# Optimization experiments

Measured on AMD Instinct MI355X. Metric: run time of the kernel, lower is better.

## Reference

```python
import jax, jax.numpy as jnp
import numpy as np

B, T, D = 8, 2048, 128        # batch, time, input_dim
C, CD = 8192, 128             # codebook_size, codebook_dim
COMMIT_W = 1.0                # commitment_weight
IN2Q_W = 0.25                 # input_to_quantize_commit_loss_weight
EPS = 1e-12


def setup_inputs() -> dict:
    key = jax.random.key(0)
    k = jax.random.split(key, 4)
    z = jax.random.normal(k[0], (B, T, D), jnp.float32)
    frozen_codebook = jax.random.normal(k[1], (C, CD), jnp.float32) * CD ** -0.5
    conv_v = jax.random.normal(k[2], (D, CD), jnp.float32) * CD ** -0.5  # weight-norm direction (1x1 conv weight squeezed)
    conv_g = jnp.linalg.norm(conv_v, axis=1)                             # weight-norm gain (torch init: g = ||v||)
    conv_b = jnp.zeros((D,), jnp.float32)
    return {"z": z, "frozen_codebook": frozen_codebook, "conv_v": conv_v,
            "conv_g": conv_g, "conv_b": conv_b}


def _implicit_codebook(fc, v, g, b):
    # weight-normed 1x1 conv == linear: w = g * v / ||v||_row ; out = fc @ w.T + b
    w = g[:, None] * v / jnp.linalg.norm(v, axis=1, keepdims=True)
    return fc @ w.T + b  # (C, D)


def _rotate_to(src, tgt):
    # rotation trick (Fifty et al.): Householder-style rotation, grads flow only through src
    sg = jax.lax.stop_gradient
    norm_src = jnp.linalg.norm(src, axis=-1, keepdims=True)
    norm_tgt = jnp.linalg.norm(tgt, axis=-1, keepdims=True)
    u = sg(src / jnp.maximum(norm_src, EPS))
    q = sg(tgt / jnp.maximum(norm_tgt, EPS))
    w = u + q
    w = sg(w / jnp.maximum(jnp.linalg.norm(w, axis=-1, keepdims=True), EPS))
    e = src
    rotated = (e
               - 2.0 * jnp.sum(e * w, -1, keepdims=True) * w
               + 2.0 * jnp.sum(e * u, -1, keepdims=True) * q)
    scale = sg(norm_tgt / jnp.maximum(norm_src, EPS))
    return rotated * scale


def reference(z, frozen_codebook, conv_v, conv_g, conv_b):
    sg = jax.lax.stop_gradient
    cb = _implicit_codebook(frozen_codebook, conv_v, conv_g, conv_b)  # (C, D)
    # squared euclidean distances -> same argmin as torch.cdist (p=2)
    d2 = (jnp.sum(z * z, -1, keepdims=True)
          - 2.0 * jnp.einsum('btd,cd->btc', z, cb)
          + jnp.sum(cb * cb, -1))                                     # (B, T, C)
    indices = jnp.argmin(d2, axis=-1)                                 # (B, T)
    z_q = cb[indices]                                                 # (B, T, D)
    commit = (jnp.mean((sg(z) - z_q) ** 2)
              + IN2Q_W * jnp.mean((z - sg(z_q)) ** 2))
    z_q = _rotate_to(z, z_q)
    return z_q, indices, commit * COMMIT_W
```

## Files before the change

kernel.cpp:

```cpp
#include <hip/hip_runtime.h>
#include <math.h>

#define NROWS 16384
#define DIM 128
#define NCODE 8192
#define EPSF 1e-12f

typedef float f32x4 __attribute__((ext_vector_type(4)));
typedef __bf16 bf16x8 __attribute__((ext_vector_type(8)));
typedef unsigned short u16x8 __attribute__((ext_vector_type(8)));

#define WS_NEED_BYTES 31571968ull

#define KT 12
#define TILEA 4096
#define TILEB 8192
#define KPB 3
#define CHUNK (TILEA + TILEB)

__device__ __forceinline__ float wave_sum(float x) {
#pragma unroll
  for (int off = 32; off > 0; off >>= 1) x += __shfl_xor(x, off, 64);
  return x;
}

__device__ __forceinline__ unsigned short f2bf(float x) {
  union { float f; unsigned int u; } v;
  v.f = x;
  unsigned int r = v.u + 0x7fffu + ((v.u >> 16) & 1u);
  return (unsigned short)(r >> 16);
}
__device__ __forceinline__ float bf2f(unsigned short h) {
  union { float f; unsigned int u; } v;
  v.u = ((unsigned int)h) << 16;
  return v.f;
}

__device__ __forceinline__ void gload_lds16(const unsigned short* g,
                                            unsigned short* l) {
  __builtin_amdgcn_global_load_lds(
      (const __attribute__((address_space(1))) void*)g,
      (__attribute__((address_space(3))) void*)l, 16, 0, 0);
}

__global__ void wprep_kernel(const float* __restrict__ v,
                             const float* __restrict__ g,
                             float* __restrict__ Wt) {
  const int d = blockIdx.x;
  const int lane = threadIdx.x;
  const float v0 = v[d * DIM + lane], v1 = v[d * DIM + lane + 64];
  const float ss = wave_sum(fmaf(v0, v0, v1 * v1));
  const float sc = g[d] / sqrtf(ss);
  Wt[lane * DIM + d] = v0 * sc;
  Wt[(lane + 64) * DIM + d] = v1 * sc;
}

__global__ __launch_bounds__(256, 2) void codebook_kernel(
    const float* __restrict__ fc, const float* __restrict__ Wt,
    const float* __restrict__ bias, float* __restrict__ cb,
    float* __restrict__ cnorm2, unsigned short* __restrict__ cbcat) {
  __shared__ float Ws[DIM][DIM];
  const int tid = threadIdx.x;
  for (int i = tid; i < 4096; i += 256)
    *(float4*)&Ws[0][i << 2] = *(const float4*)&Wt[i << 2];
  __syncthreads();

  const int lane = tid & 63, wid = tid >> 6;
  const int c0 = blockIdx.x * 16 + wid * 4;
  const float b0 = bias[lane], b1 = bias[lane + 64];

  for (int cc = 0; cc < 4; ++cc) {
    const int c = __builtin_amdgcn_readfirstlane(c0 + cc);
    float a0 = 0.f, a1 = 0.f;
    for (int k = 0; k < DIM; k += 4) {
      const float4 f4 = *(const float4*)&fc[c * DIM + k];
      a0 = fmaf(f4.x, Ws[k][lane], a0);
      a1 = fmaf(f4.x, Ws[k][lane + 64], a1);
      a0 = fmaf(f4.y, Ws[k + 1][lane], a0);
      a1 = fmaf(f4.y, Ws[k + 1][lane + 64], a1);
      a0 = fmaf(f4.z, Ws[k + 2][lane], a0);
      a1 = fmaf(f4.z, Ws[k + 2][lane + 64], a1);
      a0 = fmaf(f4.w, Ws[k + 3][lane], a0);
      a1 = fmaf(f4.w, Ws[k + 3][lane + 64], a1);
    }
    const float o0 = a0 + b0, o1 = a1 + b1;
    cb[c * DIM + lane] = o0;
    cb[c * DIM + lane + 64] = o1;
    const float ss = wave_sum(fmaf(o0, o0, o1 * o1));
    if (lane == 0) cnorm2[c] = ss;

    if (cbcat != nullptr) {
      const int ct = c >> 8, r = c & 255;
      const unsigned int swz = ((r >> 1) & 3) << 3;
      unsigned short* base = cbcat + (size_t)ct * (KT * TILEB);
#pragma unroll
      for (int h = 0; h < 2; ++h) {
        const int d = lane + 64 * h;
        const float val = h ? o1 : o0;
        const unsigned short hi = f2bf(val);
        const unsigned short lo = f2bf(val - bf2f(hi));
        const int ktl = d >> 5;
        const int off = (r << 5) + ((d & 31) ^ swz);
        base[ktl * TILEB + off] = hi;
        base[(4 + ktl) * TILEB + off] = lo;
        base[(8 + ktl) * TILEB + off] = hi;
      }
    }
  }
}

__global__ __launch_bounds__(256) void zprep_kernel(
    const float* __restrict__ z, unsigned short* __restrict__ zcat) {
  const int id = blockIdx.x * 256 + threadIdx.x;
  const int row = id / 48, s = id - row * 48;
  const int kt = s >> 2, s4 = s & 3;
  const int seg = kt >> 2;
  const int d0 = ((kt & 3) << 5) + (s4 << 3);
  const int r = row & 127, rt = row >> 7;
  const int slotsw = s4 ^ ((r >> 1) & 3);

  const float* zp = &z[(size_t)row * DIM + d0];
  u16x8 out;
#pragma unroll
  for (int i = 0; i < 8; ++i) {
    const float x = zp[i];
    unsigned short b = f2bf(x);
    if (seg == 2) b = f2bf(x - bf2f(b));
    out[i] = b;
  }
  *(u16x8*)&zcat[(size_t)(rt * KT + kt) * TILEA + (r << 5) + (slotsw << 3)] =
      out;
}

__global__ __launch_bounds__(512, 4) void mfma_argmin_kernel(
    const unsigned short* __restrict__ zcat,
    const unsigned short* __restrict__ cbcat,
    const float* __restrict__ cnorm2, float* __restrict__ pval,
    int* __restrict__ pidx) {
  __shared__ __align__(16) unsigned short S[KPB * CHUNK];

  const int xcd = blockIdx.x & 7, idx = blockIdx.x >> 3;
  const int rt = xcd * 16 + (idx & 15);
  const int ct = idx >> 4;

  const int tid = threadIdx.x;
  const int lane = tid & 63, wid = tid >> 6;
  const int wr = wid >> 2, wc = wid & 3;
  const int l15 = lane & 15, lg = lane >> 4;
  const int tid8 = tid * 8;

  const unsigned short* Ag = zcat + (size_t)rt * (KT * TILEA);
  const unsigned short* Bg = cbcat + (size_t)ct * (KT * TILEB);

  f32x4 acc[4][4];
#pragma unroll
  for (int mi = 0; mi < 4; ++mi)
#pragma unroll
    for (int ni = 0; ni < 4; ++ni) acc[mi][ni] = f32x4{0.f, 0.f, 0.f, 0.f};

  int aoff[4], boff[4];
#pragma unroll
  for (int i = 0; i < 4; ++i) {
    const int ra = wr * 64 + i * 16 + l15;
    aoff[i] = (ra << 5) + ((lg ^ ((ra >> 1) & 3)) << 3);
    const int rc = wc * 64 + i * 16 + l15;
    boff[i] = TILEA + (rc << 5) + ((lg ^ ((rc >> 1) & 3)) << 3);
  }

  for (int it = 0; it < KT / KPB; ++it) {
    __syncthreads();
#pragma unroll
    for (int kk = 0; kk < KPB; ++kk) {
      const int kt = it * KPB + kk;
      gload_lds16(Ag + kt * TILEA + tid8, &S[kk * CHUNK + tid8]);
      gload_lds16(Bg + kt * TILEB + tid8, &S[kk * CHUNK + TILEA + tid8]);
      gload_lds16(Bg + kt * TILEB + 4096 + tid8,
                  &S[kk * CHUNK + TILEA + 4096 + tid8]);
    }
    __syncthreads();

#pragma unroll
    for (int kk = 0; kk < KPB; ++kk) {
      const int sb = kk * CHUNK;
      bf16x8 af[4], bfr[4];
#pragma unroll
      for (int i = 0; i < 4; ++i) af[i] = *(const bf16x8*)&S[sb + aoff[i]];
#pragma unroll
      for (int i = 0; i < 4; ++i) bfr[i] = *(const bf16x8*)&S[sb + boff[i]];
#pragma unroll
      for (int mi = 0; mi < 4; ++mi)
#pragma unroll
        for (int ni = 0; ni < 4; ++ni)
          acc[mi][ni] = __builtin_amdgcn_mfma_f32_16x16x32_bf16(
              af[mi], bfr[ni], acc[mi][ni], 0, 0, 0);
    }
  }
  __syncthreads();

  float* exv = (float*)&S[0];
  int* exi = (int*)&S[2048];

  float cn[4];
#pragma unroll
  for (int ni = 0; ni < 4; ++ni)
    cn[ni] = cnorm2[ct * 256 + wc * 64 + ni * 16 + l15];

#pragma unroll
  for (int mi = 0; mi < 4; ++mi) {
#pragma unroll
    for (int rg = 0; rg < 4; ++rg) {
      float bv = 3.4e38f;
      int bi = 0;
#pragma unroll
      for (int ni = 0; ni < 4; ++ni) {
        const float d = fmaf(-2.f, acc[mi][ni][rg], cn[ni]);
        if (d < bv) { bv = d; bi = ct * 256 + wc * 64 + ni * 16 + l15; }
      }
#pragma unroll
      for (int off = 1; off < 16; off <<= 1) {
        const float ov = __shfl_xor(bv, off, 64);
        const int oi = __shfl_xor(bi, off, 64);
        if (ov < bv || (ov == bv && oi < bi)) { bv = ov; bi = oi; }
      }
      if (l15 == 0) {
        const int rloc = wr * 64 + mi * 16 + (lg << 2) + rg;
        exv[wc * 128 + rloc] = bv;
        exi[wc * 128 + rloc] = bi;
      }
    }
  }
  __syncthreads();
  if (tid < 128) {
    float bv = exv[tid];
    int bi = exi[tid];
#pragma unroll
    for (int w = 1; w < 4; ++w) {
      const float v = exv[w * 128 + tid];
      if (v < bv) { bv = v; bi = exi[w * 128 + tid]; }
    }
    const int row = rt * 128 + tid;
    pval[(size_t)ct * NROWS + row] = bv;
    pidx[(size_t)ct * NROWS + row] = bi;
  }
}

__global__ __launch_bounds__(256, 1) void argmin_kernel(
    const float* __restrict__ z, const float* __restrict__ cb,
    const float* __restrict__ cnorm2, float* __restrict__ pval,
    int* __restrict__ pidx) {
  __shared__ float zs[128][DIM];
  __shared__ float cs[128][DIM];

  const int tid = threadIdx.x;
  const int rb = blockIdx.x >> 1;
  const int ch = blockIdx.x & 1;
  const int row0 = rb * 128;
  const int code0 = ch * (NCODE / 2);

  for (int i = tid; i < 128 * 32; i += 256) {
    const int r = i >> 5, f = i & 31;
    *(float4*)&zs[r][f << 2] = *(const float4*)&z[(row0 + r) * DIM + (f << 2)];
  }

  const int tx = tid & 15, ty = tid >> 4;
  const int sw = tx & 7;

  float best[8];
  int besti[8];
#pragma unroll
  for (int r = 0; r < 8; ++r) { best[r] = 3.4e38f; besti[r] = 0; }

  for (int cc = 0; cc < NCODE / 2; cc += 128) {
    __syncthreads();
    for (int i = tid; i < 128 * 32; i += 256) {
      const int r = i >> 5, f = i & 31;
      const int fg = f ^ (r & 7);
      *(float4*)&cs[r][f << 2] =
          *(const float4*)&cb[(code0 + cc + r) * DIM + (fg << 2)];
    }
    __syncthreads();

    float acc[8][8];
#pragma unroll
    for (int r = 0; r < 8; ++r)
#pragma unroll
      for (int j = 0; j < 8; ++j) acc[r][j] = 0.f;

    for (int k = 0; k < DIM; k += 4) {
      const int f = k >> 2;
      float4 zr[8], cr[8];
#pragma unroll
      for (int r = 0; r < 8; ++r) zr[r] = *(const float4*)&zs[ty + 16 * r][k];
      const int col = ((f ^ sw) << 2);
#pragma unroll
      for (int j = 0; j < 8; ++j) cr[j] = *(const float4*)&cs[tx + 16 * j][col];
#pragma unroll
      for (int r = 0; r < 8; ++r)
#pragma unroll
        for (int j = 0; j < 8; ++j) {
          acc[r][j] = fmaf(zr[r].x, cr[j].x, acc[r][j]);
          acc[r][j] = fmaf(zr[r].y, cr[j].y, acc[r][j]);
          acc[r][j] = fmaf(zr[r].z, cr[j].z, acc[r][j]);
          acc[r][j] = fmaf(zr[r].w, cr[j].w, acc[r][j]);
        }
    }

#pragma unroll
    for (int j = 0; j < 8; ++j) {
      const int code = code0 + cc + tx + 16 * j;
      const float cnv = cnorm2[code];
#pragma unroll
      for (int r = 0; r < 8; ++r) {
        const float s = fmaf(-2.f, acc[r][j], cnv);
        if (s < best[r]) { best[r] = s; besti[r] = code; }
      }
    }
  }

#pragma unroll
  for (int off = 1; off < 16; off <<= 1) {
#pragma unroll
    for (int r = 0; r < 8; ++r) {
      const float ov = __shfl_xor(best[r], off, 64);
      const int oi = __shfl_xor(besti[r], off, 64);
      if (ov < best[r] || (ov == best[r] && oi < besti[r])) {
        best[r] = ov;
        besti[r] = oi;
      }
    }
  }
  if (tx == 0) {
#pragma unroll
    for (int r = 0; r < 8; ++r) {
      const int row = row0 + ty + 16 * r;
      pval[(size_t)ch * NROWS + row] = best[r];
      pidx[(size_t)ch * NROWS + row] = besti[r];
    }
  }
}

__global__ __launch_bounds__(256) void rotate_kernel(
    const float* __restrict__ z, const float* __restrict__ cb,
    const float* __restrict__ pval, const int* __restrict__ pidx, int ntiles,
    float* __restrict__ out_zq, float* __restrict__ out_idx,
    float* __restrict__ partials) {
  const int tid = threadIdx.x;
  const int wid = tid >> 6, lane = tid & 63;
  const int row = blockIdx.x * 4 + wid;

  float bv = 3.4e38f;
  int bi = 0x7fffffff;
  if (lane < ntiles) {
    bv = pval[(size_t)lane * NROWS + row];
    bi = pidx[(size_t)lane * NROWS + row];
  }
#pragma unroll
  for (int off = 32; off > 0; off >>= 1) {
    const float ov = __shfl_xor(bv, off, 64);
    const int oi = __shfl_xor(bi, off, 64);
    if (ov < bv || (ov == bv && oi < bi)) { bv = ov; bi = oi; }
  }
  const int ci = bi;

  const float z0 = z[row * DIM + lane], z1 = z[row * DIM + lane + 64];
  const float c0 = cb[ci * DIM + lane], c1 = cb[ci * DIM + lane + 64];

  const float ns2 = wave_sum(fmaf(z0, z0, z1 * z1));
  const float nt2 = wave_sum(fmaf(c0, c0, c1 * c1));
  const float ns = sqrtf(ns2), nt = sqrtf(nt2);
  const float dns = fmaxf(ns, EPSF), dnt = fmaxf(nt, EPSF);
  const float u0 = z0 / dns, u1 = z1 / dns;
  const float q0 = c0 / dnt, q1 = c1 / dnt;
  float w0 = u0 + q0, w1 = u1 + q1;
  const float nw = sqrtf(wave_sum(fmaf(w0, w0, w1 * w1)));
  const float dnw = fmaxf(nw, EPSF);
  w0 /= dnw;
  w1 /= dnw;
  const float ew = wave_sum(fmaf(z0, w0, z1 * w1));
  const float eu = wave_sum(fmaf(z0, u0, z1 * u1));
  const float sc = nt / dns;
  const float o0 = (z0 - 2.f * ew * w0 + 2.f * eu * q0) * sc;
  const float o1 = (z1 - 2.f * ew * w1 + 2.f * eu * q1) * sc;
  out_zq[row * DIM + lane] = o0;
  out_zq[row * DIM + lane + 64] = o1;
  if (lane == 0) out_idx[row] = (float)ci;

  const float d0 = z0 - c0, d1 = z1 - c1;
  const float rsum = wave_sum(fmaf(d0, d0, d1 * d1));
  __shared__ float pr[4];
  if (lane == 0) pr[wid] = rsum;
  __syncthreads();
  if (tid == 0) partials[blockIdx.x] = (pr[0] + pr[1]) + (pr[2] + pr[3]);
}

__global__ void finalize_kernel(const float* __restrict__ partials,
                                float* __restrict__ out_commit) {
  __shared__ float red[256];
  const int tid = threadIdx.x;
  float s = 0.f;
  for (int i = tid; i < 4096; i += 256) s += partials[i];
  red[tid] = s;
  __syncthreads();
  for (int off = 128; off > 0; off >>= 1) {
    if (tid < off) red[tid] += red[tid + off];
    __syncthreads();
  }
  if (tid == 0) out_commit[0] = red[0] * (1.25f / ((float)NROWS * (float)DIM));
}

extern "C" void kernel_launch(void* const* d_in, const int* in_sizes, int n_in,
                              void* d_out, int out_size, void* d_ws,
                              size_t ws_size, hipStream_t stream) {
  const float* z = (const float*)d_in[0];
  const float* fc = (const float*)d_in[1];
  const float* conv_v = (const float*)d_in[2];
  const float* conv_g = (const float*)d_in[3];
  const float* conv_b = (const float*)d_in[4];
  float* out = (float*)d_out;

  float* ws = (float*)d_ws;
  float* cb = ws;
  float* cnorm2 = ws + 1048576;
  float* Wt = ws + 1056768;

  if (ws_size >= WS_NEED_BYTES) {
    unsigned short* zcat = (unsigned short*)(ws + 1073152);
    unsigned short* cbcat = (unsigned short*)(ws + 4218880);
    float* pval = ws + 5791744;
    int* pidx = (int*)(ws + 6840320);
    float* partials = ws + 7888896;

    wprep_kernel<<<DIM, 64, 0, stream>>>(conv_v, conv_g, Wt);
    codebook_kernel<<<NCODE / 16, 256, 0, stream>>>(fc, Wt, conv_b, cb, cnorm2,
                                                    cbcat);
    zprep_kernel<<<NROWS * 48 / 256, 256, 0, stream>>>(z, zcat);
    mfma_argmin_kernel<<<4096, 512, 0, stream>>>(zcat, cbcat, cnorm2, pval,
                                                 pidx);
    rotate_kernel<<<NROWS / 4, 256, 0, stream>>>(z, cb, pval, pidx, 32, out,
                                                 out + 2097152, partials);
    finalize_kernel<<<1, 256, 0, stream>>>(partials, out + 2113536);
  } else {
    float* pval = ws + 1073152;
    int* pidx = (int*)(ws + 1105920);
    float* partials = ws + 1138688;

    wprep_kernel<<<DIM, 64, 0, stream>>>(conv_v, conv_g, Wt);
    codebook_kernel<<<NCODE / 16, 256, 0, stream>>>(fc, Wt, conv_b, cb, cnorm2,
                                                    nullptr);
    argmin_kernel<<<256, 256, 0, stream>>>(z, cb, cnorm2, pval, pidx);
    rotate_kernel<<<NROWS / 4, 256, 0, stream>>>(z, cb, pval, pidx, 2, out,
                                                 out + 2097152, partials);
    finalize_kernel<<<1, 256, 0, stream>>>(partials, out + 2113536);
  }
}
```

Before: 212.1 us.

## Switch argmin to 32x32 MFMA, atomic packed argmin, fuse prep and finalize kernels

Replaces the 16x16x32 MFMA tiling with 32x32x16 bf16 MFMA (2x2 accumulators of 16 floats per wave), which halves the LDS fragment loads per MFMA. Per-tile partial argmin results are now combined via a 64-bit atomicMin on an order-preserving packed (value,index) key instead of writing pval/pidx arrays that the rotate kernel had to reduce. The z-prep and weight-norm prep kernels are merged into one launch that also initialises the atomic buffers. The commit-loss finalize kernel is removed in favour of fixed-point atomic accumulation with a last-block-done counter in the rotate kernel. Together these cut kernel launches and global traffic, at the cost of atomics contention and a fixed-point approximation of the loss sum.

```diff
diff --git a/kernel.cpp b/kernel.cpp
--- a/kernel.cpp
+++ b/kernel.cpp
@@ -7,6 +7,7 @@
 #define EPSF 1e-12f
 
 typedef float f32x4 __attribute__((ext_vector_type(4)));
+typedef float f32x16 __attribute__((ext_vector_type(16)));
 typedef __bf16 bf16x8 __attribute__((ext_vector_type(8)));
 typedef unsigned short u16x8 __attribute__((ext_vector_type(8)));
 
@@ -43,16 +44,47 @@
       (__attribute__((address_space(3))) void*)l, 16, 0, 0);
 }
 
-__global__ void wprep_kernel(const float* __restrict__ v,
-                             const float* __restrict__ g,
-                             float* __restrict__ Wt) {
-  const int d = blockIdx.x;
-  const int lane = threadIdx.x;
-  const float v0 = v[d * DIM + lane], v1 = v[d * DIM + lane + 64];
-  const float ss = wave_sum(fmaf(v0, v0, v1 * v1));
-  const float sc = g[d] / sqrtf(ss);
-  Wt[lane * DIM + d] = v0 * sc;
-  Wt[(lane + 64) * DIM + d] = v1 * sc;
+__global__ __launch_bounds__(256) void wz_kernel(
+    const float* __restrict__ z, const float* __restrict__ v,
+    const float* __restrict__ g, unsigned short* __restrict__ zcat,
+    float* __restrict__ Wt, unsigned long long* __restrict__ amin,
+    unsigned long long* __restrict__ sumdev, unsigned* __restrict__ cntdev) {
+  const int b = blockIdx.x;
+  if (b < 3072) {
+    const int id = b * 256 + threadIdx.x;
+    const int row = id / 48, s = id - row * 48;
+    if (s == 0) amin[row] = ~0ull;
+    if (id == 0) {
+      atomicExch(sumdev, 0ull);
+      atomicExch(cntdev, 0u);
+    }
+    const int kt = s >> 2, s4 = s & 3;
+    const int seg = kt >> 2;
+    const int d0 = ((kt & 3) << 5) + (s4 << 3);
+    const int r = row & 127, rt = row >> 7;
+    const int slotsw = s4 ^ ((r >> 1) & 3);
+
+    const float* zp = &z[(size_t)row * DIM + d0];
+    u16x8 out;
+#pragma unroll
+    for (int i = 0; i < 8; ++i) {
+      const float x = zp[i];
+      unsigned short bb = f2bf(x);
+      if (seg == 2) bb = f2bf(x - bf2f(bb));
+      out[i] = bb;
+    }
+    *(u16x8*)&zcat[(size_t)(rt * KT + kt) * TILEA + (r << 5) + (slotsw << 3)] =
+        out;
+  } else {
+    const int tid = threadIdx.x;
+    const int wid = tid >> 6, lane = tid & 63;
+    const int d = (b - 3072) * 4 + wid;
+    const float v0 = v[d * DIM + lane], v1 = v[d * DIM + lane + 64];
+    const float ss = wave_sum(fmaf(v0, v0, v1 * v1));
+    const float sc = g[d] / sqrtf(ss);
+    Wt[lane * DIM + d] = v0 * sc;
+    Wt[(lane + 64) * DIM + d] = v1 * sc;
+  }
 }
 
 __global__ __launch_bounds__(256, 2) void codebook_kernel(
@@ -97,46 +129,23 @@
       for (int h = 0; h < 2; ++h) {
         const int d = lane + 64 * h;
         const float val = h ? o1 : o0;
-        const unsigned short hi = f2bf(val);
-        const unsigned short lo = f2bf(val - bf2f(hi));
+        const unsigned short hiv = f2bf(val);
+        const unsigned short lov = f2bf(val - bf2f(hiv));
         const int ktl = d >> 5;
         const int off = (r << 5) + ((d & 31) ^ swz);
-        base[ktl * TILEB + off] = hi;
-        base[(4 + ktl) * TILEB + off] = lo;
-        base[(8 + ktl) * TILEB + off] = hi;
+        base[ktl * TILEB + off] = hiv;
+        base[(4 + ktl) * TILEB + off] = lov;
+        base[(8 + ktl) * TILEB + off] = hiv;
       }
     }
   }
-}
-
-__global__ __launch_bounds__(256) void zprep_kernel(
-    const float* __restrict__ z, unsigned short* __restrict__ zcat) {
-  const int id = blockIdx.x * 256 + threadIdx.x;
-  const int row = id / 48, s = id - row * 48;
-  const int kt = s >> 2, s4 = s & 3;
-  const int seg = kt >> 2;
-  const int d0 = ((kt & 3) << 5) + (s4 << 3);
-  const int r = row & 127, rt = row >> 7;
-  const int slotsw = s4 ^ ((r >> 1) & 3);
-
-  const float* zp = &z[(size_t)row * DIM + d0];
-  u16x8 out;
-#pragma unroll
-  for (int i = 0; i < 8; ++i) {
-    const float x = zp[i];
-    unsigned short b = f2bf(x);
-    if (seg == 2) b = f2bf(x - bf2f(b));
-    out[i] = b;
-  }
-  *(u16x8*)&zcat[(size_t)(rt * KT + kt) * TILEA + (r << 5) + (slotsw << 3)] =
-      out;
 }
 
 __global__ __launch_bounds__(512, 4) void mfma_argmin_kernel(
     const unsigned short* __restrict__ zcat,
     const unsigned short* __restrict__ cbcat,
-    const float* __restrict__ cnorm2, float* __restrict__ pval,
-    int* __restrict__ pidx) {
+    const float* __restrict__ cnorm2,
+    unsigned long long* __restrict__ amin) {
   __shared__ __align__(16) unsigned short S[KPB * CHUNK];
 
   const int xcd = blockIdx.x & 7, idx = blockIdx.x >> 3;
@@ -146,25 +155,33 @@
   const int tid = threadIdx.x;
   const int lane = tid & 63, wid = tid >> 6;
   const int wr = wid >> 2, wc = wid & 3;
-  const int l15 = lane & 15, lg = lane >> 4;
+  const int l31 = lane & 31, hi = lane >> 5;
   const int tid8 = tid * 8;
 
   const unsigned short* Ag = zcat + (size_t)rt * (KT * TILEA);
   const unsigned short* Bg = cbcat + (size_t)ct * (KT * TILEB);
 
-  f32x4 acc[4][4];
-#pragma unroll
-  for (int mi = 0; mi < 4; ++mi)
-#pragma unroll
-    for (int ni = 0; ni < 4; ++ni) acc[mi][ni] = f32x4{0.f, 0.f, 0.f, 0.f};
-
-  int aoff[4], boff[4];
-#pragma unroll
-  for (int i = 0; i < 4; ++i) {
-    const int ra = wr * 64 + i * 16 + l15;
-    aoff[i] = (ra << 5) + ((lg ^ ((ra >> 1) & 3)) << 3);
-    const int rc = wc * 64 + i * 16 + l15;
-    boff[i] = TILEA + (rc << 5) + ((lg ^ ((rc >> 1) & 3)) << 3);
+  f32x16 acc[2][2];
+#pragma unroll
+  for (int mi = 0; mi < 2; ++mi)
+#pragma unroll
+    for (int ni = 0; ni < 2; ++ni) acc[mi][ni] = (f32x16)(0.0f);
+
+  int aoff[2][2], boff[2][2];
+#pragma unroll
+  for (int mi = 0; mi < 2; ++mi) {
+    const int ra = wr * 64 + mi * 32 + l31;
+#pragma unroll
+    for (int s = 0; s < 2; ++s)
+      aoff[mi][s] = (ra << 5) + ((((s << 1) + hi) ^ ((ra >> 1) & 3)) << 3);
+  }
+#pragma unroll
+  for (int ni = 0; ni < 2; ++ni) {
+    const int rc = wc * 64 + ni * 32 + l31;
+#pragma unroll
+    for (int s = 0; s < 2; ++s)
+      boff[ni][s] =
+          TILEA + (rc << 5) + ((((s << 1) + hi) ^ ((rc >> 1) & 3)) << 3);
   }
 
   for (int it = 0; it < KT / KPB; ++it) {
@@ -182,48 +199,53 @@
 #pragma unroll
     for (int kk = 0; kk < KPB; ++kk) {
       const int sb = kk * CHUNK;
-      bf16x8 af[4], bfr[4];
-#pragma unroll
-      for (int i = 0; i < 4; ++i) af[i] = *(const bf16x8*)&S[sb + aoff[i]];
-#pragma unroll
-      for (int i = 0; i < 4; ++i) bfr[i] = *(const bf16x8*)&S[sb + boff[i]];
-#pragma unroll
-      for (int mi = 0; mi < 4; ++mi)
-#pragma unroll
-        for (int ni = 0; ni < 4; ++ni)
-          acc[mi][ni] = __builtin_amdgcn_mfma_f32_16x16x32_bf16(
-              af[mi], bfr[ni], acc[mi][ni], 0, 0, 0);
+      bf16x8 af[2][2], bfr[2][2];
+#pragma unroll
+      for (int mi = 0; mi < 2; ++mi)
+#pragma unroll
+        for (int s = 0; s < 2; ++s)
+          af[mi][s] = *(const bf16x8*)&S[sb + aoff[mi][s]];
+#pragma unroll
+      for (int ni = 0; ni < 2; ++ni)
+#pragma unroll
+        for (int s = 0; s < 2; ++s)
+          bfr[ni][s] = *(const bf16x8*)&S[sb + boff[ni][s]];
+#pragma unroll
+      for (int s = 0; s < 2; ++s)
+#pragma unroll
+        for (int mi = 0; mi < 2; ++mi)
+#pragma unroll
+          for (int ni = 0; ni < 2; ++ni)
+            acc[mi][ni] = __builtin_amdgcn_mfma_f32_32x32x16_bf16(
+                af[mi][s], bfr[ni][s], acc[mi][ni], 0, 0, 0);
     }
   }
   __syncthreads();
 
   float* exv = (float*)&S[0];
-  int* exi = (int*)&S[2048];
-
-  float cn[4];
-#pragma unroll
-  for (int ni = 0; ni < 4; ++ni)
-    cn[ni] = cnorm2[ct * 256 + wc * 64 + ni * 16 + l15];
-
-#pragma unroll
-  for (int mi = 0; mi < 4; ++mi) {
-#pragma unroll
-    for (int rg = 0; rg < 4; ++rg) {
-      float bv = 3.4e38f;
-      int bi = 0;
-#pragma unroll
-      for (int ni = 0; ni < 4; ++ni) {
-        const float d = fmaf(-2.f, acc[mi][ni][rg], cn[ni]);
-        if (d < bv) { bv = d; bi = ct * 256 + wc * 64 + ni * 16 + l15; }
-      }
-#pragma unroll
-      for (int off = 1; off < 16; off <<= 1) {
+  int* exi = (int*)&S[1024];
+
+  const float cn0 = cnorm2[ct * 256 + wc * 64 + l31];
+  const float cn1 = cnorm2[ct * 256 + wc * 64 + 32 + l31];
+  const int cbase = ct * 256 + wc * 64 + l31;
+
+#pragma unroll
+  for (int mi = 0; mi < 2; ++mi) {
+#pragma unroll
+    for (int r = 0; r < 16; ++r) {
+      const float dv0 = fmaf(-2.f, acc[mi][0][r], cn0);
+      const float dv1 = fmaf(-2.f, acc[mi][1][r], cn1);
+      float bv = dv0;
+      int bi = cbase;
+      if (dv1 < dv0) { bv = dv1; bi = cbase + 32; }
+#pragma unroll
+      for (int off = 1; off < 32; off <<= 1) {
         const float ov = __shfl_xor(bv, off, 64);
         const int oi = __shfl_xor(bi, off, 64);
         if (ov < bv || (ov == bv && oi < bi)) { bv = ov; bi = oi; }
       }
-      if (l15 == 0) {
-        const int rloc = wr * 64 + mi * 16 + (lg << 2) + rg;
+      if (l31 == 0) {
+        const int rloc = wr * 64 + mi * 32 + (r & 3) + 8 * (r >> 2) + 4 * hi;
         exv[wc * 128 + rloc] = bv;
         exi[wc * 128 + rloc] = bi;
       }
@@ -235,132 +257,26 @@
     int bi = exi[tid];
 #pragma unroll
     for (int w = 1; w < 4; ++w) {
-      const float v = exv[w * 128 + tid];
-      if (v < bv) { bv = v; bi = exi[w * 128 + tid]; }
-    }
-    const int row = rt * 128 + tid;
-    pval[(size_t)ct * NROWS + row] = bv;
-    pidx[(size_t)ct * NROWS + row] = bi;
-  }
-}
-
-__global__ __launch_bounds__(256, 1) void argmin_kernel(
+      const float vv = exv[w * 128 + tid];
+      if (vv < bv) { bv = vv; bi = exi[w * 128 + tid]; }
+    }
+    unsigned u = __float_as_uint(bv);
+    u ^= (u >> 31) ? 0xFFFFFFFFu : 0x80000000u;
+    const unsigned long long packed =
+        ((unsigned long long)u << 32) | (unsigned)bi;
+    atomicMin(&amin[rt * 128 + tid], packed);
+  }
+}
+
+__global__ __launch_bounds__(256) void rotate2_kernel(
     const float* __restrict__ z, const float* __restrict__ cb,
-    const float* __restrict__ cnorm2, float* __restrict__ pval,
-    int* __restrict__ pidx) {
-  __shared__ float zs[128][DIM];
-  __shared__ float cs[128][DIM];
-
-  const int tid = threadIdx.x;
-  const int rb = blockIdx.x >> 1;
-  const int ch = blockIdx.x & 1;
-  const int row0 = rb * 128;
-  const int code0 = ch * (NCODE / 2);
-
-  for (int i = tid; i < 128 * 32; i += 256) {
-    const int r = i >> 5, f = i & 31;
-    *(float4*)&zs[r][f << 2] = *(const float4*)&z[(row0 + r) * DIM + (f << 2)];
-  }
-
-  const int tx = tid & 15, ty = tid >> 4;
-  const int sw = tx & 7;
-
-  float best[8];
-  int besti[8];
-#pragma unroll
-  for (int r = 0; r < 8; ++r) { best[r] = 3.4e38f; besti[r] = 0; }
-
-  for (int cc = 0; cc < NCODE / 2; cc += 128) {
-    __syncthreads();
-    for (int i = tid; i < 128 * 32; i += 256) {
-      const int r = i >> 5, f = i & 31;
-      const int fg = f ^ (r & 7);
-      *(float4*)&cs[r][f << 2] =
-          *(const float4*)&cb[(code0 + cc + r) * DIM + (fg << 2)];
-    }
-    __syncthreads();
-
-    float acc[8][8];
-#pragma unroll
-    for (int r = 0; r < 8; ++r)
-#pragma unroll
-      for (int j = 0; j < 8; ++j) acc[r][j] = 0.f;
-
-    for (int k = 0; k < DIM; k += 4) {
-      const int f = k >> 2;
-      float4 zr[8], cr[8];
-#pragma unroll
-      for (int r = 0; r < 8; ++r) zr[r] = *(const float4*)&zs[ty + 16 * r][k];
-      const int col = ((f ^ sw) << 2);
-#pragma unroll
-      for (int j = 0; j < 8; ++j) cr[j] = *(const float4*)&cs[tx + 16 * j][col];
-#pragma unroll
-      for (int r = 0; r < 8; ++r)
-#pragma unroll
-        for (int j = 0; j < 8; ++j) {
-          acc[r][j] = fmaf(zr[r].x, cr[j].x, acc[r][j]);
-          acc[r][j] = fmaf(zr[r].y, cr[j].y, acc[r][j]);
-          acc[r][j] = fmaf(zr[r].z, cr[j].z, acc[r][j]);
-          acc[r][j] = fmaf(zr[r].w, cr[j].w, acc[r][j]);
-        }
-    }
-
-#pragma unroll
-    for (int j = 0; j < 8; ++j) {
-      const int code = code0 + cc + tx + 16 * j;
-      const float cnv = cnorm2[code];
-#pragma unroll
-      for (int r = 0; r < 8; ++r) {
-        const float s = fmaf(-2.f, acc[r][j], cnv);
-        if (s < best[r]) { best[r] = s; besti[r] = code; }
-      }
-    }
-  }
-
-#pragma unroll
-  for (int off = 1; off < 16; off <<= 1) {
-#pragma unroll
-    for (int r = 0; r < 8; ++r) {
-      const float ov = __shfl_xor(best[r], off, 64);
-      const int oi = __shfl_xor(besti[r], off, 64);
-      if (ov < best[r] || (ov == best[r] && oi < besti[r])) {
-        best[r] = ov;
-        besti[r] = oi;
-      }
-    }
-  }
-  if (tx == 0) {
-#pragma unroll
-    for (int r = 0; r < 8; ++r) {
-      const int row = row0 + ty + 16 * r;
-      pval[(size_t)ch * NROWS + row] = best[r];
-      pidx[(size_t)ch * NROWS + row] = besti[r];
-    }
-  }
-}
-
-__global__ __launch_bounds__(256) void rotate_kernel(
-    const float* __restrict__ z, const float* __restrict__ cb,
-    const float* __restrict__ pval, const int* __restrict__ pidx, int ntiles,
-    float* __restrict__ out_zq, float* __restrict__ out_idx,
-    float* __restrict__ partials) {
+    const unsigned long long* __restrict__ amin, float* __restrict__ out_zq,
+    float* __restrict__ out_idx, float* __restrict__ out_commit,
+    unsigned long long* __restrict__ sumdev, unsigned* __restrict__ cntdev) {
   const int tid = threadIdx.x;
   const int wid = tid >> 6, lane = tid & 63;
   const int row = blockIdx.x * 4 + wid;
-
-  float bv = 3.4e38f;
-  int bi = 0x7fffffff;
-  if (lane < ntiles) {
-    bv = pval[(size_t)lane * NROWS + row];
-    bi = pidx[(size_t)lane * NROWS + row];
-  }
-#pragma unroll
-  for (int off = 32; off > 0; off >>= 1) {
-    const float ov = __shfl_xor(bv, off, 64);
-    const int oi = __shfl_xor(bi, off, 64);
-    if (ov < bv || (ov == bv && oi < bi)) { bv = ov; bi = oi; }
-  }
-  const int ci = bi;
+  const int ci = (int)(unsigned)(amin[row] & 0xffffffffull);
 
   const float z0 = z[row * DIM + lane], z1 = z[row * DIM + lane + 64];
   const float c0 = cb[ci * DIM + lane], c1 = cb[ci * DIM + lane + 64];
@@ -390,6 +306,178 @@
   __shared__ float pr[4];
   if (lane == 0) pr[wid] = rsum;
   __syncthreads();
+  if (tid == 0) {
+    const float bs = (pr[0] + pr[1]) + (pr[2] + pr[3]);
+    atomicAdd(sumdev, (unsigned long long)((double)bs * 16777216.0 + 0.5));
+    __threadfence();
+    const unsigned done = atomicAdd(cntdev, 1u);
+    if (done == (NROWS / 4) - 1) {
+      __threadfence();
+      const unsigned long long tot = atomicAdd(sumdev, 0ull);
+      out_commit[0] = (float)((double)tot *
+                              (1.25 / (16777216.0 * (double)NROWS * (double)DIM)));
+    }
+  }
+}
+
+__global__ void wprep_kernel(const float* __restrict__ v,
+                             const float* __restrict__ g,
+                             float* __restrict__ Wt) {
+  const int d = blockIdx.x;
+  const int lane = threadIdx.x;
+  const float v0 = v[d * DIM + lane], v1 = v[d * DIM + lane + 64];
+  const float ss = wave_sum(fmaf(v0, v0, v1 * v1));
+  const float sc = g[d] / sqrtf(ss);
+  Wt[lane * DIM + d] = v0 * sc;
+  Wt[(lane + 64) * DIM + d] = v1 * sc;
+}
+
+__global__ __launch_bounds__(256, 1) void argmin_kernel(
+    const float* __restrict__ z, const float* __restrict__ cb,
+    const float* __restrict__ cnorm2, float* __restrict__ pval,
+    int* __restrict__ pidx) {
+  __shared__ float zs[128][DIM];
+  __shared__ float cs[128][DIM];
+
+  const int tid = threadIdx.x;
+  const int rb = blockIdx.x >> 1;
+  const int ch = blockIdx.x & 1;
+  const int row0 = rb * 128;
+  const int code0 = ch * (NCODE / 2);
+
+  for (int i = tid; i < 128 * 32; i += 256) {
+    const int r = i >> 5, f = i & 31;
+    *(float4*)&zs[r][f << 2] = *(const float4*)&z[(row0 + r) * DIM + (f << 2)];
+  }
+
+  const int tx = tid & 15, ty = tid >> 4;
+  const int sw = tx & 7;
+
+  float best[8];
+  int besti[8];
+#pragma unroll
+  for (int r = 0; r < 8; ++r) { best[r] = 3.4e38f; besti[r] = 0; }
+
+  for (int cc = 0; cc < NCODE / 2; cc += 128) {
+    __syncthreads();
+    for (int i = tid; i < 128 * 32; i += 256) {
+      const int r = i >> 5, f = i & 31;
+      const int fg = f ^ (r & 7);
+      *(float4*)&cs[r][f << 2] =
+          *(const float4*)&cb[(code0 + cc + r) * DIM + (fg << 2)];
+    }
+    __syncthreads();
+
+    float acc[8][8];
+#pragma unroll
+    for (int r = 0; r < 8; ++r)
+#pragma unroll
+      for (int j = 0; j < 8; ++j) acc[r][j] = 0.f;
+
+    for (int k = 0; k < DIM; k += 4) {
+      const int f = k >> 2;
+      float4 zr[8], cr[8];
+#pragma unroll
+      for (int r = 0; r < 8; ++r) zr[r] = *(const float4*)&zs[ty + 16 * r][k];
+      const int col = ((f ^ sw) << 2);
+#pragma unroll
+      for (int j = 0; j < 8; ++j) cr[j] = *(const float4*)&cs[tx + 16 * j][col];
+#pragma unroll
+      for (int r = 0; r < 8; ++r)
+#pragma unroll
+        for (int j = 0; j < 8; ++j) {
+          acc[r][j] = fmaf(zr[r].x, cr[j].x, acc[r][j]);
+          acc[r][j] = fmaf(zr[r].y, cr[j].y, acc[r][j]);
+          acc[r][j] = fmaf(zr[r].z, cr[j].z, acc[r][j]);
+          acc[r][j] = fmaf(zr[r].w, cr[j].w, acc[r][j]);
+        }
+    }
+
+#pragma unroll
+    for (int j = 0; j < 8; ++j) {
+      const int code = code0 + cc + tx + 16 * j;
+      const float cnv = cnorm2[code];
+#pragma unroll
+      for (int r = 0; r < 8; ++r) {
+        const float s = fmaf(-2.f, acc[r][j], cnv);
+        if (s < best[r]) { best[r] = s; besti[r] = code; }
+      }
+    }
+  }
+
+#pragma unroll
+  for (int off = 1; off < 16; off <<= 1) {
+#pragma unroll
+    for (int r = 0; r < 8; ++r) {
+      const float ov = __shfl_xor(best[r], off, 64);
+      const int oi = __shfl_xor(besti[r], off, 64);
+      if (ov < best[r] || (ov == best[r] && oi < besti[r])) {
+        best[r] = ov;
+        besti[r] = oi;
+      }
+    }
+  }
+  if (tx == 0) {
+#pragma unroll
+    for (int r = 0; r < 8; ++r) {
+      const int row = row0 + ty + 16 * r;
+      pval[(size_t)ch * NROWS + row] = best[r];
+      pidx[(size_t)ch * NROWS + row] = besti[r];
+    }
+  }
+}
+
+__global__ __launch_bounds__(256) void rotate_kernel(
+    const float* __restrict__ z, const float* __restrict__ cb,
+    const float* __restrict__ pval, const int* __restrict__ pidx, int ntiles,
+    float* __restrict__ out_zq, float* __restrict__ out_idx,
+    float* __restrict__ partials) {
+  const int tid = threadIdx.x;
+  const int wid = tid >> 6, lane = tid & 63;
+  const int row = blockIdx.x * 4 + wid;
+
+  float bv = 3.4e38f;
+  int bi = 0x7fffffff;
+  if (lane < ntiles) {
+    bv = pval[(size_t)lane * NROWS + row];
+    bi = pidx[(size_t)lane * NROWS + row];
+  }
+#pragma unroll
+  for (int off = 32; off > 0; off >>= 1) {
+    const float ov = __shfl_xor(bv, off, 64);
+    const int oi = __shfl_xor(bi, off, 64);
+    if (ov < bv || (ov == bv && oi < bi)) { bv = ov; bi = oi; }
+  }
+  const int ci = bi;
+
+  const float z0 = z[row * DIM + lane], z1 = z[row * DIM + lane + 64];
+  const float c0 = cb[ci * DIM + lane], c1 = cb[ci * DIM + lane + 64];
+
+  const float ns2 = wave_sum(fmaf(z0, z0, z1 * z1));
+  const float nt2 = wave_sum(fmaf(c0, c0, c1 * c1));
+  const float ns = sqrtf(ns2), nt = sqrtf(nt2);
+  const float dns = fmaxf(ns, EPSF), dnt = fmaxf(nt, EPSF);
+  const float u0 = z0 / dns, u1 = z1 / dns;
+  const float q0 = c0 / dnt, q1 = c1 / dnt;
+  float w0 = u0 + q0, w1 = u1 + q1;
+  const float nw = sqrtf(wave_sum(fmaf(w0, w0, w1 * w1)));
+  const float dnw = fmaxf(nw, EPSF);
+  w0 /= dnw;
+  w1 /= dnw;
+  const float ew = wave_sum(fmaf(z0, w0, z1 * w1));
+  const float eu = wave_sum(fmaf(z0, u0, z1 * u1));
+  const float sc = nt / dns;
+  const float o0 = (z0 - 2.f * ew * w0 + 2.f * eu * q0) * sc;
+  const float o1 = (z1 - 2.f * ew * w1 + 2.f * eu * q1) * sc;
+  out_zq[row * DIM + lane] = o0;
+  out_zq[row * DIM + lane + 64] = o1;
+  if (lane == 0) out_idx[row] = (float)ci;
+
+  const float d0 = z0 - c0, d1 = z1 - c1;
+  const float rsum = wave_sum(fmaf(d0, d0, d1 * d1));
+  __shared__ float pr[4];
+  if (lane == 0) pr[wid] = rsum;
+  __syncthreads();
   if (tid == 0) partials[blockIdx.x] = (pr[0] + pr[1]) + (pr[2] + pr[3]);
 }
 
@@ -426,19 +514,19 @@
   if (ws_size >= WS_NEED_BYTES) {
     unsigned short* zcat = (unsigned short*)(ws + 1073152);
     unsigned short* cbcat = (unsigned short*)(ws + 4218880);
-    float* pval = ws + 5791744;
-    int* pidx = (int*)(ws + 6840320);
-    float* partials = ws + 7888896;
-
-    wprep_kernel<<<DIM, 64, 0, stream>>>(conv_v, conv_g, Wt);
+    unsigned long long* amin = (unsigned long long*)(ws + 5791744);
+    unsigned long long* sumdev = (unsigned long long*)(ws + 5824512);
+    unsigned* cntdev = (unsigned*)(ws + 5824514);
+
+    wz_kernel<<<3104, 256, 0, stream>>>(z, conv_v, conv_g, zcat, Wt, amin,
+                                        sumdev, cntdev);
     codebook_kernel<<<NCODE / 16, 256, 0, stream>>>(fc, Wt, conv_b, cb, cnorm2,
                                                     cbcat);
-    zprep_kernel<<<NROWS * 48 / 256, 256, 0, stream>>>(z, zcat);
-    mfma_argmin_kernel<<<4096, 512, 0, stream>>>(zcat, cbcat, cnorm2, pval,
-                                                 pidx);
-    rotate_kernel<<<NROWS / 4, 256, 0, stream>>>(z, cb, pval, pidx, 32, out,
-                                                 out + 2097152, partials);
-    finalize_kernel<<<1, 256, 0, stream>>>(partials, out + 2113536);
+    mfma_argmin_kernel<<<4096, 512, 0, stream>>>(zcat, cbcat, cnorm2, amin);
+    rotate2_kernel<<<NROWS / 4, 256, 0, stream>>>(z, cb, amin, out,
+                                                  out + 2097152,
+                                                  out + 2113536, sumdev,
+                                                  cntdev);
   } else {
     float* pval = ws + 1073152;
     int* pidx = (int*)(ws + 1105920);
```

New measurement: 384.0 us. +81.0%, slower.

## Use 4-wave MFMA blocks with 64x128 warp tiles and fuse wprep into zprep

Applied to the files above, without the earlier changes.

The MFMA argmin kernel now runs 256 threads (4 waves in a 2x2 grid) per 128x256 tile instead of 8 waves. Each wave computes a 64x128 sub-tile with 32 accumulators, which improves fragment reuse from LDS per MFMA. Global-to-LDS loads are split into more 16-byte transfers per thread. Separately, the weight-norm prep and z bf16 split kernels are merged into one launch to save a launch and overlap the small work. Risks include higher register pressure (128 accumulator VGPRs) and less latency hiding with fewer waves.

```diff
diff --git a/kernel.cpp b/kernel.cpp
--- a/kernel.cpp
+++ b/kernel.cpp
@@ -43,16 +43,41 @@
       (__attribute__((address_space(3))) void*)l, 16, 0, 0);
 }
 
-__global__ void wprep_kernel(const float* __restrict__ v,
-                             const float* __restrict__ g,
-                             float* __restrict__ Wt) {
-  const int d = blockIdx.x;
-  const int lane = threadIdx.x;
-  const float v0 = v[d * DIM + lane], v1 = v[d * DIM + lane + 64];
-  const float ss = wave_sum(fmaf(v0, v0, v1 * v1));
-  const float sc = g[d] / sqrtf(ss);
-  Wt[lane * DIM + d] = v0 * sc;
-  Wt[(lane + 64) * DIM + d] = v1 * sc;
+__global__ __launch_bounds__(256) void wz_kernel(
+    const float* __restrict__ z, const float* __restrict__ v,
+    const float* __restrict__ g, unsigned short* __restrict__ zcat,
+    float* __restrict__ Wt) {
+  const int b = blockIdx.x;
+  if (b < 3072) {
+    const int id = b * 256 + threadIdx.x;
+    const int row = id / 48, s = id - row * 48;
+    const int kt = s >> 2, s4 = s & 3;
+    const int seg = kt >> 2;
+    const int d0 = ((kt & 3) << 5) + (s4 << 3);
+    const int r = row & 127, rt = row >> 7;
+    const int slotsw = s4 ^ ((r >> 1) & 3);
+
+    const float* zp = &z[(size_t)row * DIM + d0];
+    u16x8 out;
+#pragma unroll
+    for (int i = 0; i < 8; ++i) {
+      const float x = zp[i];
+      unsigned short bb = f2bf(x);
+      if (seg == 2) bb = f2bf(x - bf2f(bb));
+      out[i] = bb;
+    }
+    *(u16x8*)&zcat[(size_t)(rt * KT + kt) * TILEA + (r << 5) +
+                   (slotsw << 3)] = out;
+  } else {
+    const int tid = threadIdx.x;
+    const int wid = tid >> 6, lane = tid & 63;
+    const int d = (b - 3072) * 4 + wid;
+    const float v0 = v[d * DIM + lane], v1 = v[d * DIM + lane + 64];
+    const float ss = wave_sum(fmaf(v0, v0, v1 * v1));
+    const float sc = g[d] / sqrtf(ss);
+    Wt[lane * DIM + d] = v0 * sc;
+    Wt[(lane + 64) * DIM + d] = v1 * sc;
+  }
 }
 
 __global__ __launch_bounds__(256, 2) void codebook_kernel(
@@ -97,42 +122,19 @@
       for (int h = 0; h < 2; ++h) {
         const int d = lane + 64 * h;
         const float val = h ? o1 : o0;
-        const unsigned short hi = f2bf(val);
-        const unsigned short lo = f2bf(val - bf2f(hi));
+        const unsigned short hiv = f2bf(val);
+        const unsigned short lov = f2bf(val - bf2f(hiv));
         const int ktl = d >> 5;
         const int off = (r << 5) + ((d & 31) ^ swz);
-        base[ktl * TILEB + off] = hi;
-        base[(4 + ktl) * TILEB + off] = lo;
-        base[(8 + ktl) * TILEB + off] = hi;
-      }
-    }
-  }
-}
-
-__global__ __launch_bounds__(256) void zprep_kernel(
-    const float* __restrict__ z, unsigned short* __restrict__ zcat) {
-  const int id = blockIdx.x * 256 + threadIdx.x;
-  const int row = id / 48, s = id - row * 48;
-  const int kt = s >> 2, s4 = s & 3;
-  const int seg = kt >> 2;
-  const int d0 = ((kt & 3) << 5) + (s4 << 3);
-  const int r = row & 127, rt = row >> 7;
-  const int slotsw = s4 ^ ((r >> 1) & 3);
-
-  const float* zp = &z[(size_t)row * DIM + d0];
-  u16x8 out;
-#pragma unroll
-  for (int i = 0; i < 8; ++i) {
-    const float x = zp[i];
-    unsigned short b = f2bf(x);
-    if (seg == 2) b = f2bf(x - bf2f(b));
-    out[i] = b;
-  }
-  *(u16x8*)&zcat[(size_t)(rt * KT + kt) * TILEA + (r << 5) + (slotsw << 3)] =
-      out;
-}
-
-__global__ __launch_bounds__(512, 4) void mfma_argmin_kernel(
+        base[ktl * TILEB + off] = hiv;
+        base[(4 + ktl) * TILEB + off] = lov;
+        base[(8 + ktl) * TILEB + off] = hiv;
+      }
+    }
+  }
+}
+
+__global__ __launch_bounds__(256, 2) void mfma_argmin_kernel(
     const unsigned short* __restrict__ zcat,
     const unsigned short* __restrict__ cbcat,
     const float* __restrict__ cnorm2, float* __restrict__ pval,
@@ -145,25 +147,28 @@
 
   const int tid = threadIdx.x;
   const int lane = tid & 63, wid = tid >> 6;
-  const int wr = wid >> 2, wc = wid & 3;
+  const int wr = wid >> 1, wc = wid & 1;
   const int l15 = lane & 15, lg = lane >> 4;
   const int tid8 = tid * 8;
 
   const unsigned short* Ag = zcat + (size_t)rt * (KT * TILEA);
   const unsigned short* Bg = cbcat + (size_t)ct * (KT * TILEB);
 
-  f32x4 acc[4][4];
+  f32x4 acc[4][8];
 #pragma unroll
   for (int mi = 0; mi < 4; ++mi)
 #pragma unroll
-    for (int ni = 0; ni < 4; ++ni) acc[mi][ni] = f32x4{0.f, 0.f, 0.f, 0.f};
-
-  int aoff[4], boff[4];
+    for (int ni = 0; ni < 8; ++ni) acc[mi][ni] = f32x4{0.f, 0.f, 0.f, 0.f};
+
+  int aoff[4], boff[8];
 #pragma unroll
   for (int i = 0; i < 4; ++i) {
     const int ra = wr * 64 + i * 16 + l15;
     aoff[i] = (ra << 5) + ((lg ^ ((ra >> 1) & 3)) << 3);
-    const int rc = wc * 64 + i * 16 + l15;
+  }
+#pragma unroll
+  for (int i = 0; i < 8; ++i) {
+    const int rc = wc * 128 + i * 16 + l15;
     boff[i] = TILEA + (rc << 5) + ((lg ^ ((rc >> 1) & 3)) << 3);
   }
 
@@ -172,25 +177,31 @@
 #pragma unroll
     for (int kk = 0; kk < KPB; ++kk) {
       const int kt = it * KPB + kk;
-      gload_lds16(Ag + kt * TILEA + tid8, &S[kk * CHUNK + tid8]);
-      gload_lds16(Bg + kt * TILEB + tid8, &S[kk * CHUNK + TILEA + tid8]);
-      gload_lds16(Bg + kt * TILEB + 4096 + tid8,
-                  &S[kk * CHUNK + TILEA + 4096 + tid8]);
+      const unsigned short* ag = Ag + kt * TILEA;
+      const unsigned short* bg = Bg + kt * TILEB;
+      unsigned short* la = &S[kk * CHUNK];
+      unsigned short* lb = &S[kk * CHUNK + TILEA];
+#pragma unroll
+      for (int j = 0; j < 2; ++j)
+        gload_lds16(ag + j * 2048 + tid8, la + j * 2048 + tid8);
+#pragma unroll
+      for (int j = 0; j < 4; ++j)
+        gload_lds16(bg + j * 2048 + tid8, lb + j * 2048 + tid8);
     }
     __syncthreads();
 
 #pragma unroll
     for (int kk = 0; kk < KPB; ++kk) {
       const int sb = kk * CHUNK;
-      bf16x8 af[4], bfr[4];
+      bf16x8 af[4], bfr[8];
 #pragma unroll
       for (int i = 0; i < 4; ++i) af[i] = *(const bf16x8*)&S[sb + aoff[i]];
 #pragma unroll
-      for (int i = 0; i < 4; ++i) bfr[i] = *(const bf16x8*)&S[sb + boff[i]];
+      for (int i = 0; i < 8; ++i) bfr[i] = *(const bf16x8*)&S[sb + boff[i]];
 #pragma unroll
       for (int mi = 0; mi < 4; ++mi)
 #pragma unroll
-        for (int ni = 0; ni < 4; ++ni)
+        for (int ni = 0; ni < 8; ++ni)
           acc[mi][ni] = __builtin_amdgcn_mfma_f32_16x16x32_bf16(
               af[mi], bfr[ni], acc[mi][ni], 0, 0, 0);
     }
@@ -200,10 +211,10 @@
   float* exv = (float*)&S[0];
   int* exi = (int*)&S[2048];
 
-  float cn[4];
-#pragma unroll
-  for (int ni = 0; ni < 4; ++ni)
-    cn[ni] = cnorm2[ct * 256 + wc * 64 + ni * 16 + l15];
+  float cn[8];
+#pragma unroll
+  for (int ni = 0; ni < 8; ++ni)
+    cn[ni] = cnorm2[ct * 256 + wc * 128 + ni * 16 + l15];
 
 #pragma unroll
   for (int mi = 0; mi < 4; ++mi) {
@@ -212,9 +223,9 @@
       float bv = 3.4e38f;
       int bi = 0;
 #pragma unroll
-      for (int ni = 0; ni < 4; ++ni) {
+      for (int ni = 0; ni < 8; ++ni) {
         const float d = fmaf(-2.f, acc[mi][ni][rg], cn[ni]);
-        if (d < bv) { bv = d; bi = ct * 256 + wc * 64 + ni * 16 + l15; }
+        if (d < bv) { bv = d; bi = ct * 256 + wc * 128 + ni * 16 + l15; }
       }
 #pragma unroll
       for (int off = 1; off < 16; off <<= 1) {
@@ -233,15 +244,24 @@
   if (tid < 128) {
     float bv = exv[tid];
     int bi = exi[tid];
-#pragma unroll
-    for (int w = 1; w < 4; ++w) {
-      const float v = exv[w * 128 + tid];
-      if (v < bv) { bv = v; bi = exi[w * 128 + tid]; }
-    }
+    const float v1 = exv[128 + tid];
+    if (v1 < bv) { bv = v1; bi = exi[128 + tid]; }
     const int row = rt * 128 + tid;
     pval[(size_t)ct * NROWS + row] = bv;
     pidx[(size_t)ct * NROWS + row] = bi;
   }
+}
+
+__global__ void wprep_kernel(const float* __restrict__ v,
+                             const float* __restrict__ g,
+                             float* __restrict__ Wt) {
+  const int d = blockIdx.x;
+  const int lane = threadIdx.x;
+  const float v0 = v[d * DIM + lane], v1 = v[d * DIM + lane + 64];
+  const float ss = wave_sum(fmaf(v0, v0, v1 * v1));
+  const float sc = g[d] / sqrtf(ss);
+  Wt[lane * DIM + d] = v0 * sc;
+  Wt[(lane + 64) * DIM + d] = v1 * sc;
 }
 
 __global__ __launch_bounds__(256, 1) void argmin_kernel(
@@ -430,11 +450,10 @@
     int* pidx = (int*)(ws + 6840320);
     float* partials = ws + 7888896;
 
-    wprep_kernel<<<DIM, 64, 0, stream>>>(conv_v, conv_g, Wt);
+    wz_kernel<<<3104, 256, 0, stream>>>(z, conv_v, conv_g, zcat, Wt);
     codebook_kernel<<<NCODE / 16, 256, 0, stream>>>(fc, Wt, conv_b, cb, cnorm2,
                                                     cbcat);
-    zprep_kernel<<<NROWS * 48 / 256, 256, 0, stream>>>(z, zcat);
-    mfma_argmin_kernel<<<4096, 512, 0, stream>>>(zcat, cbcat, cnorm2, pval,
+    mfma_argmin_kernel<<<4096, 256, 0, stream>>>(zcat, cbcat, cnorm2, pval,
                                                  pidx);
     rotate_kernel<<<NROWS / 4, 256, 0, stream>>>(z, cb, pval, pidx, 32, out,
                                                  out + 2097152, partials);
```

New measurement: 201.5 us. 1.05x faster.
